# Kernel tuning notes

Hardware: AMD Instinct MI355X
Metric: run time of the kernel (lower is better)

The kernel has to match this reference:

```python
import jax, jax.numpy as jnp
import numpy as np

N_NODES = 50000
N_EDGES = 800000
IN_FEAT = 128
INTER_DIM = 128
OUT_FEAT = 128
EDGE_W_DIM = 3


def setup_inputs() -> dict:
    key = jax.random.key(0)
    ks = jax.random.split(key, 8)
    h = jax.random.normal(ks[0], (N_NODES, IN_FEAT), dtype=jnp.float32)
    edge_src = jax.random.randint(ks[1], (N_EDGES,), 0, N_NODES, dtype=jnp.int32)
    edge_dst = jax.random.randint(ks[2], (N_EDGES,), 0, N_NODES, dtype=jnp.int32)
    edge_w = jax.random.normal(ks[3], (N_EDGES, EDGE_W_DIM), dtype=jnp.float32)
    # xavier-normal-ish init, gain for relu
    gain = float(np.sqrt(2.0))
    W1 = jax.random.normal(ks[4], (INTER_DIM, IN_FEAT + EDGE_W_DIM), dtype=jnp.float32)
    W1 = W1 * (gain * np.sqrt(2.0 / (INTER_DIM + IN_FEAT + EDGE_W_DIM)))
    b1 = jnp.zeros((INTER_DIM,), dtype=jnp.float32)
    W2 = jax.random.normal(ks[5], (OUT_FEAT, IN_FEAT + INTER_DIM), dtype=jnp.float32)
    W2 = W2 * (gain * np.sqrt(2.0 / (OUT_FEAT + IN_FEAT + INTER_DIM)))
    b2 = jnp.zeros((OUT_FEAT,), dtype=jnp.float32)
    return {"h": h, "edge_src": edge_src, "edge_dst": edge_dst, "edge_w": edge_w,
            "W1": W1, "b1": b1, "W2": W2, "b2": b2}


def reference(h, edge_src, edge_dst, edge_w, W1, b1, W2, b2):
    n_nodes = h.shape[0]
    # per-edge message: concat(src node feature, edge weight) -> [E, in_feat+3]
    m = jnp.concatenate([h[edge_src], edge_w], axis=1)
    # linear1 + leaky_relu (torch default negative_slope=0.01)
    tmp = m @ W1.T + b1  # [E, inter_dim]
    tmp = jnp.where(tmp >= 0, tmp, 0.01 * tmp)
    # mean over incoming edges per destination node; zero-in-degree nodes get 0
    sums = jax.ops.segment_sum(tmp, edge_dst, num_segments=n_nodes)
    counts = jax.ops.segment_sum(jnp.ones((tmp.shape[0],), dtype=tmp.dtype),
                                 edge_dst, num_segments=n_nodes)
    h_N = sums / jnp.maximum(counts, 1.0)[:, None]  # [N, inter_dim]
    # tail: concat + linear2 + relu
    h_total = jnp.concatenate([h, h_N], axis=1)  # [N, in_feat+inter_dim]
    return jax.nn.relu(h_total @ W2.T + b2)
```

## Files before the change

### kernel.cpp

```cpp
#include <hip/hip_runtime.h>
#include <hip/hip_bf16.h>

#define N_NODES 50000
#define N_EDGES 800000
#define N_TILES 3125
#define CSR_BLOCKS 782
#define PROJ_BLOCKS 782
#define AF_BLOCKS 782
#define BUCKET_CAP 64

typedef __attribute__((ext_vector_type(8))) short short8;
typedef __attribute__((ext_vector_type(4))) float f32x4;
typedef __attribute__((ext_vector_type(2))) float fl2;

#define OFF_G     0
#define OFF_CUR   1600000
#define OFF_BKT   6400000
#define OFF_W1BP  12866384
#define OFF_BP1   12866896
#define OFF_BP2   12875088

__device__ inline unsigned bf16rne(float f) {
    unsigned u = __float_as_uint(f);
    return (u + 0x7fffu + ((u >> 16) & 1u)) >> 16;
}
__device__ inline unsigned pk2(float lo, float hi) {
    return bf16rne(lo) | (bf16rne(hi) << 16);
}
union FragU { unsigned u[4]; short8 s; uint4 v; };

template <bool HI>
__device__ inline fl2 fp8x2_dec_w(unsigned s) {
#if __has_builtin(__builtin_amdgcn_cvt_pk_f32_fp8)
    return __builtin_amdgcn_cvt_pk_f32_fp8((int)s, HI);
#else
    unsigned v = HI ? (s >> 16) : s;
    fl2 r;
    unsigned lo = v & 0xffu, h2 = (v >> 8) & 0xffu;
    unsigned blo = ((lo & 0x80u) << 24) | ((lo & 0x7fu) << 20);
    unsigned bhi = ((h2 & 0x80u) << 24) | ((h2 & 0x7fu) << 20);
    r.x = __uint_as_float(blo) * 0x1p120f;
    r.y = __uint_as_float(bhi) * 0x1p120f;
    return r;
#endif
}
__device__ inline unsigned fp8x4_enc(float a, float b, float c, float d) {
#if __has_builtin(__builtin_amdgcn_cvt_pk_fp8_f32)
    int u = __builtin_amdgcn_cvt_pk_fp8_f32(a, b, 0, false);
    u = __builtin_amdgcn_cvt_pk_fp8_f32(c, d, u, true);
    return (unsigned)u;
#else
    auto enc1 = [](float f) -> unsigned {
        unsigned u = __float_as_uint(f);
        unsigned sg = (u >> 24) & 0x80u;
        float af = fabsf(f);
        if (af < 0x1p-6f) return sg;
        if (af >= 448.f) return sg | 0x7eu;
        unsigned v = __float_as_uint(af);
        unsigned r = v + 0xFFFFFu + ((v >> 20) & 1u);
        unsigned E = r >> 23, m = (r >> 20) & 7u;
        return sg | ((E - 120u) << 3) | m;
    };
    return enc1(a) | (enc1(b) << 8) | (enc1(c) << 16) | (enc1(d) << 24);
#endif
}

__global__ __launch_bounds__(256) void repack_zero_kernel(
        const float* __restrict__ W1, const float* __restrict__ b1,
        const float* __restrict__ W2, float* __restrict__ W1bp,
        uint4* __restrict__ Bpack1, uint4* __restrict__ Bpack2,
        int* __restrict__ cursor) {
    int tid = blockIdx.x * 256 + threadIdx.x;
    if (tid < 2048) {
        int lane = tid & 63, ent = tid >> 6;
        int n = (ent & 7) * 16 + (lane & 15);
        int k0 = (ent >> 3) * 32 + ((lane >> 4) << 3);
        const float* src = W1 + n * 131 + k0;
        FragU f;
        f.u[0] = pk2(src[0], src[1]);
        f.u[1] = pk2(src[2], src[3]);
        f.u[2] = pk2(src[4], src[5]);
        f.u[3] = pk2(src[6], src[7]);
        Bpack1[ent * 64 + lane] = f.v;
    } else if (tid < 6144) {
        int t2 = tid - 2048;
        int lane = t2 & 63, ent = t2 >> 6;
        int n = (ent & 7) * 16 + (lane & 15);
        int k0 = (ent >> 3) * 32 + ((lane >> 4) << 3);
        const float* src = W2 + n * 256 + k0;
        FragU f;
        f.u[0] = pk2(src[0], src[1]);
        f.u[1] = pk2(src[2], src[3]);
        f.u[2] = pk2(src[4], src[5]);
        f.u[3] = pk2(src[6], src[7]);
        Bpack2[ent * 64 + lane] = f.v;
    }
    if (tid < 128) {
        W1bp[tid * 4 + 0] = W1[tid * 131 + 128];
        W1bp[tid * 4 + 1] = W1[tid * 131 + 129];
        W1bp[tid * 4 + 2] = W1[tid * 131 + 130];
        W1bp[tid * 4 + 3] = b1[tid];
    }
    if (tid < N_NODES) cursor[tid] = 0;
}

__global__ __launch_bounds__(256) void fused_bucket_proj(
        const int* __restrict__ esrc, const int* __restrict__ edst,
        const float* __restrict__ ew, int* __restrict__ cursor,
        uint2* __restrict__ bkt,
        const float* __restrict__ h, const uint4* __restrict__ Bpack1,
        unsigned* __restrict__ g8) {
    __shared__ float lds[64][132];
    const int role = blockIdx.x & 1;
    const int gb = blockIdx.x >> 1;

    if (role == 0) {
        const int base = gb * 1024 + threadIdx.x;
        int dst[4], src[4];
        float w0[4], w1[4], w2[4];
        bool ok[4];
        #pragma unroll
        for (int j = 0; j < 4; j++) {
            int e = base + j * 256;
            ok[j] = e < N_EDGES;
            int ce = ok[j] ? e : 0;
            dst[j] = edst[ce];
            src[j] = esrc[ce];
            w0[j] = ew[ce * 3 + 0];
            w1[j] = ew[ce * 3 + 1];
            w2[j] = ew[ce * 3 + 2];
        }
        int pos[4];
        #pragma unroll
        for (int j = 0; j < 4; j++)
            pos[j] = ok[j] ? atomicAdd(&cursor[dst[j]], 1) : BUCKET_CAP;
        #pragma unroll
        for (int j = 0; j < 4; j++) {
            if (ok[j] && pos[j] < BUCKET_CAP) {
                uint2 rec;
                rec.x = (unsigned)src[j] | (bf16rne(w0[j]) << 16);
                rec.y = bf16rne(w1[j]) | (bf16rne(w2[j]) << 16);
                bkt[(dst[j] << 6) + pos[j]] = rec;
            }
        }
        return;
    }

    const int wave = threadIdx.x >> 6;
    const int lane = threadIdx.x & 63;
    const int T = gb * 4 + wave;

    if (T < N_TILES) {
        f32x4 acc[8];
        #pragma unroll
        for (int i = 0; i < 8; i++) acc[i] = (f32x4)(0.f);

        const int row = T * 16 + (lane & 15);
        const float* hrow = h + row * 128 + ((lane >> 4) << 3);

        #pragma unroll
        for (int kt = 0; kt < 4; kt++) {
            float4 x0 = *(const float4*)(hrow + kt * 32);
            float4 x1 = *(const float4*)(hrow + kt * 32 + 4);
            FragU a;
            a.u[0] = pk2(x0.x, x0.y);
            a.u[1] = pk2(x0.z, x0.w);
            a.u[2] = pk2(x1.x, x1.y);
            a.u[3] = pk2(x1.z, x1.w);
            #pragma unroll
            for (int nt = 0; nt < 8; nt++) {
                FragU b;
                b.v = Bpack1[(kt * 8 + nt) * 64 + lane];
                acc[nt] = __builtin_amdgcn_mfma_f32_16x16x32_bf16(a.s, b.s, acc[nt], 0, 0, 0);
            }
        }
        #pragma unroll
        for (int nt = 0; nt < 8; nt++) {
            #pragma unroll
            for (int reg = 0; reg < 4; reg++) {
                int r = ((lane >> 4) << 2) + reg;
                lds[wave * 16 + r][nt * 16 + (lane & 15)] = acc[nt][reg];
            }
        }
    }
    __syncthreads();

    const int t = threadIdx.x;
    const int nodeL = t >> 2, seg = t & 3;
    const int gnode = gb * 64 + nodeL;
    if (gnode < N_NODES) {
        #pragma unroll
        for (int i = 0; i < 2; i++) {
            const float* p = &lds[nodeL][seg * 32 + i * 16];
            uint4 o;
            o.x = fp8x4_enc(p[0],  p[1],  p[2],  p[3]);
            o.y = fp8x4_enc(p[4],  p[5],  p[6],  p[7]);
            o.z = fp8x4_enc(p[8],  p[9],  p[10], p[11]);
            o.w = fp8x4_enc(p[12], p[13], p[14], p[15]);
            ((uint4*)g8)[gnode * 8 + seg * 2 + i] = o;
        }
    }
}

#define AGG_P 4
__global__ __launch_bounds__(256) void agg_final(
        const unsigned* __restrict__ g8u, const uint2* __restrict__ bkt,
        const int* __restrict__ cursor, const float* __restrict__ W1bp,
        const float* __restrict__ h, const uint4* __restrict__ Bpack2,
        const float* __restrict__ b2, float* __restrict__ out) {
    __shared__ __align__(16) unsigned ldsN[4][16 * 64];
    const int wave = threadIdx.x >> 6;
    const int lane = threadIdx.x & 63;
    const int half = lane >> 5;
    const int c = lane & 31;
    int T = blockIdx.x * 4 + wave;
    const bool live = (T < N_TILES);
    if (!live) T = 0;

    const float4 w0 = ((const float4*)W1bp)[4 * c + 0];
    const float4 w1 = ((const float4*)W1bp)[4 * c + 1];
    const float4 w2 = ((const float4*)W1bp)[4 * c + 2];
    const float4 w3 = ((const float4*)W1bp)[4 * c + 3];
    const fl2 cx0 = {w0.x, w1.x}, cx1 = {w2.x, w3.x};
    const fl2 cy0 = {w0.y, w1.y}, cy1 = {w2.y, w3.y};
    const fl2 cz0 = {w0.z, w1.z}, cz1 = {w2.z, w3.z};
    const fl2 cb0 = {w0.w, w1.w}, cb1 = {w2.w, w3.w};
    const fl2 kP = (fl2)(0.505f);
    const fl2 kA = (fl2)(0.495f);

    unsigned* myl = ldsN[wave];

#define EDGE_BODY(R, GV, SP, SA)                                                       \
    do {                                                                               \
        fl2 ry = (fl2)(__uint_as_float((R).x & 0xffff0000u));                          \
        fl2 rz = (fl2)(__uint_as_float((R).y << 16));                                  \
        fl2 rw = (fl2)(__uint_as_float((R).y & 0xffff0000u));                          \
        fl2 t0 = fp8x2_dec_w<false>(GV) + cb0;                                         \
        t0 = __builtin_elementwise_fma(cx0, ry, t0);                                   \
        t0 = __builtin_elementwise_fma(cy0, rz, t0);                                   \
        t0 = __builtin_elementwise_fma(cz0, rw, t0);                                   \
        acc0 = __builtin_elementwise_fma(SP, t0, acc0);                                \
        acc0 = __builtin_elementwise_fma(SA, __builtin_elementwise_abs(t0), acc0);     \
        fl2 t1 = fp8x2_dec_w<true>(GV) + cb1;                                          \
        t1 = __builtin_elementwise_fma(cx1, ry, t1);                                   \
        t1 = __builtin_elementwise_fma(cy1, rz, t1);                                   \
        t1 = __builtin_elementwise_fma(cz1, rw, t1);                                   \
        acc1 = __builtin_elementwise_fma(SP, t1, acc1);                                \
        acc1 = __builtin_elementwise_fma(SA, __builtin_elementwise_abs(t1), acc1);     \
    } while (0)

    for (int n = 0; n < 16; n++) {
        const int v = T * 16 + n;
        const int degT = cursor[v];
        const int deg = (degT < BUCKET_CAP) ? degT : BUCKET_CAP;
        const int beg = v << 6;
        const int end = beg + deg;
        fl2 acc0 = (fl2)(0.f), acc1 = (fl2)(0.f);

        int i = beg;
        for (; i + 2 * AGG_P <= end; i += 2 * AGG_P) {
            uint2 r[AGG_P];
            #pragma unroll
            for (int u = 0; u < AGG_P; u++) r[u] = bkt[i + 2 * u + half];
            unsigned gv[AGG_P];
            #pragma unroll
            for (int u = 0; u < AGG_P; u++) gv[u] = g8u[(r[u].x & 0xffffu) * 32 + c];
            #pragma unroll
            for (int u = 0; u < AGG_P; u++) EDGE_BODY(r[u], gv[u], kP, kA);
        }
        for (; i + 2 <= end; i += 2) {
            uint2 r = bkt[i + half];
            unsigned gv = g8u[(r.x & 0xffffu) * 32 + c];
            EDGE_BODY(r, gv, kP, kA);
        }
        if (i < end) {
            float sc = (half == 0) ? 1.f : 0.f;
            fl2 sP = (fl2)(0.505f * sc), sA = (fl2)(0.495f * sc);
            uint2 r = bkt[i];
            unsigned gv = g8u[(r.x & 0xffffu) * 32 + c];
            EDGE_BODY(r, gv, sP, sA);
        }

        acc0.x += __shfl_xor(acc0.x, 32);
        acc0.y += __shfl_xor(acc0.y, 32);
        acc1.x += __shfl_xor(acc1.x, 32);
        acc1.y += __shfl_xor(acc1.y, 32);
        if (half == 0) {
            float inv = 1.0f / (float)((degT > 0) ? degT : 1);
            uint2 p;
            p.x = pk2(acc0.x * inv, acc0.y * inv);
            p.y = pk2(acc1.x * inv, acc1.y * inv);
            const int idx = (2 * c) ^ ((n & 7) << 2);
            *(uint2*)&myl[n * 64 + idx] = p;
        }
    }
#undef EDGE_BODY
    __syncthreads();

    f32x4 acc[8];
    #pragma unroll
    for (int i = 0; i < 8; i++) acc[i] = (f32x4)(0.f);

    const int row = T * 16 + (lane & 15);
    const int koff = (lane >> 4) << 3;
    const float* hrow = h + row * 128 + koff;

    #pragma unroll
    for (int kt = 0; kt < 8; kt++) {
        FragU a;
        if (kt < 4) {
            float4 x0 = *(const float4*)(hrow + kt * 32);
            float4 x1 = *(const float4*)(hrow + kt * 32 + 4);
            a.u[0] = pk2(x0.x, x0.y);
            a.u[1] = pk2(x0.z, x0.w);
            a.u[2] = pk2(x1.x, x1.y);
            a.u[3] = pk2(x1.z, x1.w);
        } else {
            const int nn = lane & 15;
            const int idx = (((kt - 4) << 4) + (koff >> 1)) ^ ((nn & 7) << 2);
            a.v = *(const uint4*)&myl[nn * 64 + idx];
        }
        #pragma unroll
        for (int nt = 0; nt < 8; nt++) {
            FragU b;
            b.v = Bpack2[(kt * 8 + nt) * 64 + lane];
            acc[nt] = __builtin_amdgcn_mfma_f32_16x16x32_bf16(a.s, b.s, acc[nt], 0, 0, 0);
        }
    }
    if (live) {
        #pragma unroll
        for (int nt = 0; nt < 8; nt++) {
            int ch = nt * 16 + (lane & 15);
            float bias = b2[ch];
            #pragma unroll
            for (int reg = 0; reg < 4; reg++) {
                int node = T * 16 + ((lane >> 4) << 2) + reg;
                out[node * 128 + ch] = fmaxf(acc[nt][reg] + bias, 0.f);
            }
        }
    }
}

extern "C" void kernel_launch(void* const* d_in, const int* in_sizes, int n_in,
                              void* d_out, int out_size, void* d_ws, size_t ws_size,
                              hipStream_t stream) {
    const float* h    = (const float*)d_in[0];
    const int*   esrc = (const int*)d_in[1];
    const int*   edst = (const int*)d_in[2];
    const float* ew   = (const float*)d_in[3];
    const float* W1   = (const float*)d_in[4];
    const float* b1   = (const float*)d_in[5];
    const float* W2   = (const float*)d_in[6];
    const float* b2   = (const float*)d_in[7];
    float* out = (float*)d_out;
    float* ws  = (float*)d_ws;

    unsigned* g8  = (unsigned*)(ws + OFF_G);
    int* cursor   = (int*)(ws + OFF_CUR);
    float* W1bp   = ws + OFF_W1BP;
    uint4* Bpack1 = (uint4*)(ws + OFF_BP1);
    uint4* Bpack2 = (uint4*)(ws + OFF_BP2);
    uint2* bkt    = (uint2*)(ws + OFF_BKT);

    repack_zero_kernel<<<196, 256, 0, stream>>>(W1, b1, W2, W1bp, Bpack1, Bpack2, cursor);

    fused_bucket_proj<<<CSR_BLOCKS + PROJ_BLOCKS, 256, 0, stream>>>(
        esrc, edst, ew, cursor, bkt, h, Bpack1, g8);

    agg_final<<<AF_BLOCKS, 256, 0, stream>>>(g8, bkt, cursor, W1bp, h, Bpack2, b2, out);
}
```

Before: 199.0 us.

## Split each 16-node tile across four waves in agg_final

The aggregation+output kernel used to give each wave a whole 16-node tile, with 782 blocks of 4 tiles each. Now each block handles one tile: each wave aggregates 4 nodes into a shared LDS tile, then computes 2 of the 8 output column groups with MFMA. This launches 3125 blocks and spreads the work more finely for better occupancy and load balance. In exchange, each wave reloads the same h rows for the A fragments, so redundant h reads rise fourfold, and every block needs a barrier.

```diff
diff --git a/kernel.cpp b/kernel.cpp
--- a/kernel.cpp
+++ b/kernel.cpp
@@ -6,7 +6,6 @@
 #define N_TILES 3125
 #define CSR_BLOCKS 782
 #define PROJ_BLOCKS 782
-#define AF_BLOCKS 782
 #define BUCKET_CAP 64
 
 typedef __attribute__((ext_vector_type(8))) short short8;
@@ -208,14 +207,12 @@
         const int* __restrict__ cursor, const float* __restrict__ W1bp,
         const float* __restrict__ h, const uint4* __restrict__ Bpack2,
         const float* __restrict__ b2, float* __restrict__ out) {
-    __shared__ __align__(16) unsigned ldsN[4][16 * 64];
+    __shared__ __align__(16) unsigned ldsN[16 * 64];
     const int wave = threadIdx.x >> 6;
     const int lane = threadIdx.x & 63;
     const int half = lane >> 5;
     const int c = lane & 31;
-    int T = blockIdx.x * 4 + wave;
-    const bool live = (T < N_TILES);
-    if (!live) T = 0;
+    const int T = blockIdx.x;
 
     const float4 w0 = ((const float4*)W1bp)[4 * c + 0];
     const float4 w1 = ((const float4*)W1bp)[4 * c + 1];
@@ -227,8 +224,6 @@
     const fl2 cb0 = {w0.w, w1.w}, cb1 = {w2.w, w3.w};
     const fl2 kP = (fl2)(0.505f);
     const fl2 kA = (fl2)(0.495f);
-
-    unsigned* myl = ldsN[wave];
 
 #define EDGE_BODY(R, GV, SP, SA)                                                       \
     do {                                                                               \
@@ -249,7 +244,9 @@
         acc1 = __builtin_elementwise_fma(SA, __builtin_elementwise_abs(t1), acc1);     \
     } while (0)
 
-    for (int n = 0; n < 16; n++) {
+    #pragma unroll 1
+    for (int nl = 0; nl < 4; nl++) {
+        const int n = wave * 4 + nl;
         const int v = T * 16 + n;
         const int degT = cursor[v];
         const int deg = (degT < BUCKET_CAP) ? degT : BUCKET_CAP;
@@ -291,15 +288,15 @@
             p.x = pk2(acc0.x * inv, acc0.y * inv);
             p.y = pk2(acc1.x * inv, acc1.y * inv);
             const int idx = (2 * c) ^ ((n & 7) << 2);
-            *(uint2*)&myl[n * 64 + idx] = p;
+            *(uint2*)&ldsN[n * 64 + idx] = p;
         }
     }
 #undef EDGE_BODY
     __syncthreads();
 
-    f32x4 acc[8];
-    #pragma unroll
-    for (int i = 0; i < 8; i++) acc[i] = (f32x4)(0.f);
+    f32x4 acc[2];
+    acc[0] = (f32x4)(0.f);
+    acc[1] = (f32x4)(0.f);
 
     const int row = T * 16 + (lane & 15);
     const int koff = (lane >> 4) << 3;
@@ -318,25 +315,25 @@
         } else {
             const int nn = lane & 15;
             const int idx = (((kt - 4) << 4) + (koff >> 1)) ^ ((nn & 7) << 2);
-            a.v = *(const uint4*)&myl[nn * 64 + idx];
-        }
-        #pragma unroll
-        for (int nt = 0; nt < 8; nt++) {
+            a.v = *(const uint4*)&ldsN[nn * 64 + idx];
+        }
+        #pragma unroll
+        for (int j = 0; j < 2; j++) {
+            const int nt = wave * 2 + j;
             FragU b;
             b.v = Bpack2[(kt * 8 + nt) * 64 + lane];
-            acc[nt] = __builtin_amdgcn_mfma_f32_16x16x32_bf16(a.s, b.s, acc[nt], 0, 0, 0);
-        }
-    }
-    if (live) {
-        #pragma unroll
-        for (int nt = 0; nt < 8; nt++) {
-            int ch = nt * 16 + (lane & 15);
-            float bias = b2[ch];
-            #pragma unroll
-            for (int reg = 0; reg < 4; reg++) {
-                int node = T * 16 + ((lane >> 4) << 2) + reg;
-                out[node * 128 + ch] = fmaxf(acc[nt][reg] + bias, 0.f);
-            }
+            acc[j] = __builtin_amdgcn_mfma_f32_16x16x32_bf16(a.s, b.s, acc[j], 0, 0, 0);
+        }
+    }
+    #pragma unroll
+    for (int j = 0; j < 2; j++) {
+        const int nt = wave * 2 + j;
+        const int ch = nt * 16 + (lane & 15);
+        const float bias = b2[ch];
+        #pragma unroll
+        for (int reg = 0; reg < 4; reg++) {
+            const int node = T * 16 + ((lane >> 4) << 2) + reg;
+            out[node * 128 + ch] = fmaxf(acc[j][reg] + bias, 0.f);
         }
     }
 }
@@ -367,5 +364,5 @@
     fused_bucket_proj<<<CSR_BLOCKS + PROJ_BLOCKS, 256, 0, stream>>>(
         esrc, edst, ew, cursor, bkt, h, Bpack1, g8);
 
-    agg_final<<<AF_BLOCKS, 256, 0, stream>>>(g8, bkt, cursor, W1bp, h, Bpack2, b2, out);
-}
+    agg_final<<<N_TILES, 256, 0, stream>>>(g8, bkt, cursor, W1bp, h, Bpack2, b2, out);
+}
```

Result: slower. 205.6 us (+3.3%).
